# Optimization experiments

Hardware: AMD Instinct MI355X
Metric: run time of the kernel (lower is better)

## Reference

```python
import jax, jax.numpy as jnp
import numpy as np

B, T, F, D, NH, HD, WIN = 4, 512, 32, 128, 4, 32, 64
HIDDEN = 4 * D


def _ln(x, g, b, eps=1e-5):
    m = x.mean(-1, keepdims=True)
    v = ((x - m) ** 2).mean(-1, keepdims=True)
    return (x - m) / jnp.sqrt(v + eps) * g + b


def _rope(x):
    # x: [N, T, NH, HD] -- identical rotary applied to every head (matches per-head loop)
    hd = x.shape[-1]
    inv_freq = 1.0 / (10000.0 ** (jnp.arange(0, hd, 2, dtype=jnp.float32) / hd))
    t = jnp.arange(x.shape[1], dtype=jnp.float32)
    fr = t[:, None] * inv_freq                      # [T, HD/2]
    sin = jnp.sin(fr)[None, :, None, :]
    cos = jnp.cos(fr)[None, :, None, :]
    xe, xo = x[..., 0::2], x[..., 1::2]
    re = xe * cos - xo * sin
    ro = xe * sin + xo * cos
    return jnp.stack([re, ro], axis=-1).reshape(x.shape)


def setup_inputs() -> dict:
    key = jax.random.key(0)
    ks = jax.random.split(key, 8)
    s = 0.05
    return {
        "x": jax.random.normal(ks[0], (B, T, F), jnp.float32),
        "W_in": jax.random.normal(ks[1], (D, F), jnp.float32) * s,
        "b_in": jnp.zeros((D,), jnp.float32),
        "gamma1": jnp.ones((D,), jnp.float32),
        "beta1": jnp.zeros((D,), jnp.float32),
        "gamma2": jnp.ones((D,), jnp.float32),
        "beta2": jnp.zeros((D,), jnp.float32),
        "W_qkv": jax.random.normal(ks[2], (3 * D, D), jnp.float32) * s,
        "b_qkv": jnp.zeros((3 * D,), jnp.float32),
        "W_o": jax.random.normal(ks[3], (D, D), jnp.float32) * s,
        "b_o": jnp.zeros((D,), jnp.float32),
        "W1": jax.random.normal(ks[4], (HIDDEN, D), jnp.float32) * s,
        "b1": jnp.zeros((HIDDEN,), jnp.float32),
        "W2": jax.random.normal(ks[5], (D, HIDDEN), jnp.float32) * s,
        "b2": jnp.zeros((D,), jnp.float32),
        "W_out": jax.random.normal(ks[6], (F, D), jnp.float32) * s,
        "b_out": jnp.zeros((F,), jnp.float32),
    }


def reference(x, W_in, b_in, gamma1, beta1, gamma2, beta2, W_qkv, b_qkv,
              W_o, b_o, W1, b1, W2, b2, W_out, b_out):
    Bb, Tt, Ff = x.shape
    # channel-independent projection: hcf[b,f,t,:] = x[b,t,f] * W_in[:,f] + b_in
    hcf = jnp.einsum('btf,df->bftd', x, W_in) + b_in        # [B,F,T,D]
    hcf = hcf.reshape(Bb * Ff, Tt, D)                       # [BF,T,D]
    h1 = _ln(hcf, gamma1, beta1)
    # RoPE on q,k BEFORE the attention's internal qkv projection (as in source)
    qk = _rope(h1.reshape(Bb * Ff, Tt, NH, HD)).reshape(Bb * Ff, Tt, D)
    Wq, Wk, Wv = jnp.split(W_qkv, 3, axis=0)
    bq, bk, bv = jnp.split(b_qkv, 3)
    Q = (qk @ Wq.T + bq).reshape(-1, Tt, NH, HD)
    K = (qk @ Wk.T + bk).reshape(-1, Tt, NH, HD)
    V = (h1 @ Wv.T + bv).reshape(-1, Tt, NH, HD)
    i = jnp.arange(Tt)
    allowed = (i[None, :] <= i[:, None]) & ((i[:, None] - i[None, :]) <= WIN)
    mask = jnp.where(allowed, 0.0, -jnp.inf)                # [T,T]
    scores = jnp.einsum('bthd,bshd->bhts', Q, K) / jnp.sqrt(jnp.float32(HD)) + mask
    p = jax.nn.softmax(scores, axis=-1)
    o = jnp.einsum('bhts,bshd->bthd', p, V).reshape(-1, Tt, D)
    y = o @ W_o.T + b_o
    h2 = hcf + y
    h3 = _ln(h2, gamma2, beta2)
    ffn = jax.nn.gelu(h3 @ W1.T + b1, approximate=False) @ W2.T + b2
    h4 = h2 + ffn
    y_out = h4.reshape(Bb, Ff, Tt, D).mean(-1).transpose(0, 2, 1)   # [B,T,F]
    y_proj = (x @ W_in.T + b_in) @ W_out.T + b_out                   # [B,T,F]
    return x + y_out + y_proj
```

## Files before the change

kernel.cpp:

```cpp
#include <hip/hip_runtime.h>
#include <hip/hip_bf16.h>

typedef unsigned short u16;
typedef unsigned int u32;
typedef __attribute__((ext_vector_type(8))) short bf16x8;
typedef __attribute__((ext_vector_type(4))) float f32x4;
typedef __attribute__((ext_vector_type(4))) unsigned short u16x4;
typedef __attribute__((ext_vector_type(2))) unsigned int u32x2;

static constexpr int TSEQ = 512;
static constexpr int NSEQ = 128;
static constexpr int NTOK = NSEQ * TSEQ;

__device__ __forceinline__ float bf2f(u16 u) {
  u32 i = ((u32)u) << 16; float f; __builtin_memcpy(&f, &i, 4); return f;
}
__device__ __forceinline__ u16 f2bf(float f) {
  u32 u; __builtin_memcpy(&u, &f, 4);
  return (u16)((u + 0x7FFFu + ((u >> 16) & 1u)) >> 16);
}
__device__ __forceinline__ f32x4 mfma16(bf16x8 a, bf16x8 b, f32x4 c) {
  return __builtin_amdgcn_mfma_f32_16x16x32_bf16(a, b, c, 0, 0, 0);
}
__device__ __forceinline__ void gload_lds16(const u16* g, u16* l) {
  __builtin_amdgcn_global_load_lds((const __attribute__((address_space(1))) void*)g,
                                   (__attribute__((address_space(3))) void*)l, 16, 0, 0);
}
__device__ __forceinline__ float gelu_t(float v) {
  float uu = 0.7978845608f * (v + 0.044715f * v * v * v);
  return v / (1.f + __expf(-2.f * uu));
}

__global__ void k0_prep(const float* __restrict__ Wqkv, const float* __restrict__ Wo,
                        const float* __restrict__ W1, const float* __restrict__ W2,
                        const float* __restrict__ b2,
                        u16* __restrict__ Wqkv_b, u16* __restrict__ Wo_b,
                        u16* __restrict__ W1_b, float* __restrict__ cm,
                        float* __restrict__ b2m,
                        float* __restrict__ rc, float* __restrict__ rs) {
  int i = blockIdx.x * 256 + threadIdx.x;
  if (i < 49152) Wqkv_b[i] = f2bf(Wqkv[i]);
  if (i < 16384) Wo_b[i] = f2bf(Wo[i]);
  if (i < 65536) W1_b[i] = f2bf(W1[i]);
  if (i < 512) {
    float s = 0.f;
    for (int d = 0; d < 128; ++d) s += W2[d * 512 + i];
    cm[i] = s * (1.f / 128.f);
  }
  if (i == 0) {
    float s = 0.f;
    for (int d = 0; d < 128; ++d) s += b2[d];
    *b2m = s * (1.f / 128.f);
  }
  if (i < 8192) {
    int t = i >> 4, fi = i & 15;
    float inv = powf(10000.f, -(float)(2 * fi) / 32.f);
    float ang = (float)t * inv;
    rc[i] = cosf(ang); rs[i] = sinf(ang);
  }
}

__global__ void k1_embed(const float* __restrict__ x, const float* __restrict__ W_in,
                         const float* __restrict__ b_in,
                         const float* __restrict__ g1, const float* __restrict__ be1,
                         u16* __restrict__ hcf, u16* __restrict__ h1, u16* __restrict__ qk,
                         const float* __restrict__ rc, const float* __restrict__ rs) {
  int w = threadIdx.x >> 6, l = threadIdx.x & 63;
  int n = blockIdx.x * 4 + w;
  int t = n & (TSEQ - 1), seq = n >> 9;
  int f = seq & 31, b = seq >> 5;
  float xv = x[((b << 9) + t) * 32 + f];
  int d0 = l * 2;
  float v0 = xv * W_in[d0 * 32 + f] + b_in[d0];
  float v1 = xv * W_in[(d0 + 1) * 32 + f] + b_in[d0 + 1];
  float s = v0 + v1, ss = v0 * v0 + v1 * v1;
  #pragma unroll
  for (int m = 1; m < 64; m <<= 1) { s += __shfl_xor(s, m); ss += __shfl_xor(ss, m); }
  float mean = s * (1.f / 128.f);
  float var = ss * (1.f / 128.f) - mean * mean;
  float rstd = rsqrtf(var + 1e-5f);
  float a0 = (v0 - mean) * rstd * g1[d0] + be1[d0];
  float a1 = (v1 - mean) * rstd * g1[d0 + 1] + be1[d0 + 1];
  ((u32*)hcf)[n * 64 + l] = (u32)f2bf(v0) | ((u32)f2bf(v1) << 16);
  ((u32*)h1)[n * 64 + l]  = (u32)f2bf(a0) | ((u32)f2bf(a1) << 16);
  float c = rc[t * 16 + (l & 15)], sn = rs[t * 16 + (l & 15)];
  float re = a0 * c - a1 * sn, ro = a0 * sn + a1 * c;
  ((u32*)qk)[n * 64 + l] = (u32)f2bf(re) | ((u32)f2bf(ro) << 16);
}

__global__ __launch_bounds__(512, 4)
void gemm_qkv(const u16* __restrict__ QKin, const u16* __restrict__ H1,
              const u16* __restrict__ Wqkv, const float* __restrict__ bqkv,
              u16* __restrict__ QKb, u16* __restrict__ Vb) {
  __shared__ u16 Aq[64 * 128];
  __shared__ u16 Ah[64 * 128];
  const int tid = threadIdx.x, l = tid & 63, w = tid >> 6;
  const int lr = l & 15, lg = l >> 4;
  const int m0 = blockIdx.x * 64;
  const int wb = __builtin_amdgcn_readfirstlane(tid & 0x1C0);

  #pragma unroll
  for (int it = 0; it < 2; ++it) {
    int ci = it * 512 + tid;
    int row = ci >> 4, p = ci & 15;
    size_t goff = (size_t)(m0 + row) * 128 + ((p ^ (row & 7)) << 3);
    gload_lds16(QKin + goff, Aq + (size_t)(it * 512 + wb) * 8);
    gload_lds16(H1 + goff, Ah + (size_t)(it * 512 + wb) * 8);
  }
  __syncthreads();

  #pragma unroll 1
  for (int ph = 0; ph < 3; ++ph) {
    const u16* As = (ph == 2) ? Ah : Aq;
    const int wrow = ph * 128 + w * 16;
    const u16* wr = Wqkv + (size_t)(wrow + lr) * 128 + lg * 8;
    bf16x8 wf0 = *(const bf16x8*)(wr);
    bf16x8 wf1 = *(const bf16x8*)(wr + 32);
    bf16x8 wf2 = *(const bf16x8*)(wr + 64);
    bf16x8 wf3 = *(const bf16x8*)(wr + 96);
    f32x4 bs = *(const f32x4*)(bqkv + wrow + lg * 4);
    u16* C = (ph == 2) ? Vb : QKb;
    const int ldc = (ph == 2) ? 128 : 256;
    const int ccol = ((ph == 2) ? 0 : ph * 128) + w * 16 + lg * 4;
    #pragma unroll
    for (int tt = 0; tt < 4; ++tt) {
      const int tok = tt * 16 + lr;
      const u16* ar = As + (tok * 16) * 8;
      f32x4 a0 = mfma16(wf0, *(const bf16x8*)(ar + ((lg ^ (lr & 7)) << 3)),
                        (f32x4){0.f, 0.f, 0.f, 0.f});
      a0 = mfma16(wf1, *(const bf16x8*)(ar + (((4 + lg) ^ (lr & 7)) << 3)), a0);
      f32x4 a1 = mfma16(wf2, *(const bf16x8*)(ar + (((8 + lg) ^ (lr & 7)) << 3)),
                        (f32x4){0.f, 0.f, 0.f, 0.f});
      a1 = mfma16(wf3, *(const bf16x8*)(ar + (((12 + lg) ^ (lr & 7)) << 3)), a1);
      f32x4 a = a0 + a1;
      u16x4 qv;
      #pragma unroll
      for (int r = 0; r < 4; ++r) qv[r] = f2bf(a[r] + bs[r]);
      *(u16x4*)(C + (size_t)(m0 + tok) * ldc + ccol) = qv;
    }
    __builtin_amdgcn_sched_barrier(0);
  }
}

__global__ __launch_bounds__(512, 4)
void wo_ln_ffn(const u16* __restrict__ OB, const u16* __restrict__ Wo_b,
               const float* __restrict__ bo, const u16* __restrict__ HCF,
               const float* __restrict__ g2, const float* __restrict__ be2,
               const u16* __restrict__ W1b, const float* __restrict__ b1,
               const float* __restrict__ cm, const float* __restrict__ b2m,
               float* __restrict__ yout) {
  __shared__ u16 Buf[64 * 136];
  __shared__ float Sm[64 * 8], Sq[64 * 8];
  __shared__ float Yp[64 * 8];
  __shared__ float Hm[64];
  const int tid = threadIdx.x, l = tid & 63, w = tid >> 6;
  const int lr = l & 15, lg = l >> 4;
  const int m0 = blockIdx.x * 64;
  const int wb = __builtin_amdgcn_readfirstlane(tid & 0x1C0);

  #pragma unroll
  for (int it = 0; it < 2; ++it) {
    int ci = it * 512 + tid;
    int row = ci >> 4, p = ci & 15;
    gload_lds16(OB + (size_t)(m0 + row) * 128 + ((p ^ (row & 7)) << 3),
                Buf + (size_t)(it * 512 + wb) * 8);
  }
  __syncthreads();

  const int wrow = w * 16;
  {
    const u16* wr0 = Wo_b + (size_t)(wrow + lr) * 128 + lg * 8;
    bf16x8 wf0 = *(const bf16x8*)(wr0);
    bf16x8 wf1 = *(const bf16x8*)(wr0 + 32);
    bf16x8 wf2 = *(const bf16x8*)(wr0 + 64);
    bf16x8 wf3 = *(const bf16x8*)(wr0 + 96);
    f32x4 bs = *(const f32x4*)(bo + wrow + lg * 4);
    f32x4 hv[4];
    #pragma unroll
    for (int tt = 0; tt < 4; ++tt) {
      const int tok = tt * 16 + lr;
      const u16* ar = Buf + (tok * 16) * 8;
      f32x4 a0 = mfma16(wf0, *(const bf16x8*)(ar + ((lg ^ (lr & 7)) << 3)),
                        (f32x4){0.f, 0.f, 0.f, 0.f});
      a0 = mfma16(wf1, *(const bf16x8*)(ar + (((4 + lg) ^ (lr & 7)) << 3)), a0);
      f32x4 a1 = mfma16(wf2, *(const bf16x8*)(ar + (((8 + lg) ^ (lr & 7)) << 3)),
                        (f32x4){0.f, 0.f, 0.f, 0.f});
      a1 = mfma16(wf3, *(const bf16x8*)(ar + (((12 + lg) ^ (lr & 7)) << 3)), a1);
      f32x4 a = a0 + a1;
      u16x4 rv = *(const u16x4*)(HCF + (size_t)(m0 + tok) * 128 + wrow + lg * 4);
      #pragma unroll
      for (int r = 0; r < 4; ++r) hv[tt][r] = a[r] + bs[r] + bf2f(rv[r]);
    }
    #pragma unroll
    for (int tt = 0; tt < 4; ++tt) {
      float psm = hv[tt][0] + hv[tt][1] + hv[tt][2] + hv[tt][3];
      float psq = hv[tt][0] * hv[tt][0] + hv[tt][1] * hv[tt][1]
                + hv[tt][2] * hv[tt][2] + hv[tt][3] * hv[tt][3];
      psm += __shfl_xor(psm, 16); psq += __shfl_xor(psq, 16);
      psm += __shfl_xor(psm, 32); psq += __shfl_xor(psq, 32);
      if (lg == 0) { Sm[(tt * 16 + lr) * 8 + w] = psm; Sq[(tt * 16 + lr) * 8 + w] = psq; }
    }
    __syncthreads();
    f32x4 gm = *(const f32x4*)(g2 + wrow + lg * 4);
    f32x4 bt = *(const f32x4*)(be2 + wrow + lg * 4);
    #pragma unroll
    for (int tt = 0; tt < 4; ++tt) {
      const int tok = tt * 16 + lr;
      float s = 0.f, q = 0.f;
      #pragma unroll
      for (int ww = 0; ww < 8; ++ww) { s += Sm[tok * 8 + ww]; q += Sq[tok * 8 + ww]; }
      float mean = s * (1.f / 128.f);
      float var = q * (1.f / 128.f) - mean * mean;
      float rstd = rsqrtf(var + 1e-5f);
      if (w == 0 && lg == 0) Hm[tok] = mean;
      u16x4 qv;
      #pragma unroll
      for (int r = 0; r < 4; ++r)
        qv[r] = f2bf((hv[tt][r] - mean) * rstd * gm[r] + bt[r]);
      *(u16x4*)(Buf + tok * 136 + wrow + lg * 4) = qv;
    }
  }
  __syncthreads();

  float yacc[4] = {0.f, 0.f, 0.f, 0.f};
  #pragma unroll 1
  for (int p = 0; p < 4; ++p) {
    const int hb = (p * 8 + w) * 16;
    const u16* wr = W1b + (size_t)(hb + lr) * 128 + lg * 8;
    bf16x8 wf0 = *(const bf16x8*)(wr);
    bf16x8 wf1 = *(const bf16x8*)(wr + 32);
    bf16x8 wf2 = *(const bf16x8*)(wr + 64);
    bf16x8 wf3 = *(const bf16x8*)(wr + 96);
    f32x4 cmv = *(const f32x4*)(cm + hb + lg * 4);
    f32x4 bsv = *(const f32x4*)(b1 + hb + lg * 4);
    #pragma unroll
    for (int tt = 0; tt < 4; ++tt) {
      const u16* ar = Buf + (tt * 16 + lr) * 136 + lg * 8;
      f32x4 a0 = mfma16(wf0, *(const bf16x8*)(ar), (f32x4){0.f, 0.f, 0.f, 0.f});
      a0 = mfma16(wf1, *(const bf16x8*)(ar + 32), a0);
      f32x4 a1 = mfma16(wf2, *(const bf16x8*)(ar + 64), (f32x4){0.f, 0.f, 0.f, 0.f});
      a1 = mfma16(wf3, *(const bf16x8*)(ar + 96), a1);
      f32x4 a = a0 + a1;
      #pragma unroll
      for (int r = 0; r < 4; ++r)
        yacc[tt] += cmv[r] * gelu_t(a[r] + bsv[r]);
    }
    __builtin_amdgcn_sched_barrier(0);
  }

  #pragma unroll
  for (int tt = 0; tt < 4; ++tt) {
    float p = yacc[tt];
    p += __shfl_xor(p, 16);
    p += __shfl_xor(p, 32);
    if (lg == 0) Yp[(tt * 16 + lr) * 8 + w] = p;
  }
  __syncthreads();
  if (tid < 64) {
    float s = 0.f;
    #pragma unroll
    for (int ww = 0; ww < 8; ++ww) s += Yp[tid * 8 + ww];
    yout[m0 + tid] = Hm[tid] + b2m[0] + s;
  }
}

__global__ __launch_bounds__(256, 4)
void attn_mfma(const u16* __restrict__ QK, const u16* __restrict__ V, u16* __restrict__ O) {
  __shared__ u16 Ks[192 * 32];
  __shared__ u16 Vt[32 * 192];
  __shared__ u16 Pl[4][16 * 96];
  const int qstart = blockIdx.x * 128, seq = blockIdx.y, h = blockIdx.z;
  const int tid = threadIdx.x, w = tid >> 6, l = tid & 63;
  const int lr = l & 15, lg = l >> 4;
  const size_t base = (size_t)seq * TSEQ;

  #pragma unroll
  for (int it = 0; it < 3; ++it) {
    int idx = it * 256 + tid;
    int kl = idx >> 2, c = idx & 3;
    int kg = qstart - 64 + kl; if (kg < 0) kg = 0;
    bf16x8 kv = *(const bf16x8*)(QK + (base + kg) * 256 + 128 + h * 32 + c * 8);
    int pc = c ^ ((kl >> 1) & 3);
    *(bf16x8*)(Ks + kl * 32 + pc * 8) = kv;
    bf16x8 vv = *(const bf16x8*)(V + (base + kg) * 128 + h * 32 + c * 8);
    #pragma unroll
    for (int j = 0; j < 8; ++j) {
      int hd = c * 8 + j;
      int f = ((hd & 7) ^ (hd >> 3)) & 7;
      Vt[hd * 192 + (((kl >> 3) ^ f) * 8) + (kl & 7)] = (u16)vv[j];
    }
  }
  __syncthreads();

  const float scale = 0.17677669529663687f;
  for (int qt = 0; qt < 2; ++qt) {
    const int klbase = (w * 2 + qt) * 16;
    const int t0 = qstart + klbase;
    bf16x8 qf = *(const bf16x8*)(QK + (base + t0 + lr) * 256 + h * 32 + lg * 8);
    f32x4 s[5];
    #pragma unroll
    for (int kt = 0; kt < 5; ++kt) {
      int key = klbase + kt * 16 + lr;
      int pc = lg ^ ((key >> 1) & 3);
      bf16x8 kf = *(const bf16x8*)(Ks + key * 32 + pc * 8);
      s[kt] = mfma16(kf, qf, (f32x4){0.f, 0.f, 0.f, 0.f});
    }
    float m = -1e30f;
    #pragma unroll
    for (int kt = 0; kt < 5; ++kt)
      #pragma unroll
      for (int r = 0; r < 4; ++r) {
        int kl = kt * 16 + lg * 4 + r;
        bool valid = (kl >= lr) && (kl <= lr + 64) && (kl >= 64 - t0);
        float sv = valid ? s[kt][r] * scale : -1e30f;
        s[kt][r] = sv;
        m = fmaxf(m, sv);
      }
    m = fmaxf(m, __shfl_xor(m, 16));
    m = fmaxf(m, __shfl_xor(m, 32));
    float sum = 0.f;
    #pragma unroll
    for (int kt = 0; kt < 5; ++kt)
      #pragma unroll
      for (int r = 0; r < 4; ++r) { float p = __expf(s[kt][r] - m); s[kt][r] = p; sum += p; }
    sum += __shfl_xor(sum, 16);
    sum += __shfl_xor(sum, 32);
    float rinv = 1.f / sum;
    u16* P = Pl[w];
    #pragma unroll
    for (int kt = 0; kt < 5; ++kt) {
      u32 lo = (u32)f2bf(s[kt][0] * rinv) | ((u32)f2bf(s[kt][1] * rinv) << 16);
      u32 hi = (u32)f2bf(s[kt][2] * rinv) | ((u32)f2bf(s[kt][3] * rinv) << 16);
      int u = 2 * kt + (lg >> 1);
      int up = (u & ~3) | ((u & 3) ^ (lr & 3));
      *(u32x2*)(P + lr * 96 + up * 8 + (lg & 1) * 4) = (u32x2){lo, hi};
    }
    {
      int u = 10 + (lg >> 1);
      int up = (u & ~3) | ((u & 3) ^ (lr & 3));
      *(u32x2*)(P + lr * 96 + up * 8 + (lg & 1) * 4) = (u32x2){0u, 0u};
    }
    f32x4 acc[2] = {{0.f,0.f,0.f,0.f},{0.f,0.f,0.f,0.f}};
    #pragma unroll
    for (int c = 0; c < 3; ++c) {
      int u = 4 * c + (lg ^ (lr & 3));
      bf16x8 pf = *(const bf16x8*)(P + lr * 96 + u * 8);
      #pragma unroll
      for (int n = 0; n < 2; ++n) {
        int hd = n * 16 + lr;
        int f = ((hd & 7) ^ (hd >> 3)) & 7;
        int uv = (klbase >> 3) + 4 * c + lg; if (uv > 23) uv = 23;
        bf16x8 vf = *(const bf16x8*)(Vt + hd * 192 + ((uv ^ f) * 8));
        acc[n] = mfma16(pf, vf, acc[n]);
      }
    }
    #pragma unroll
    for (int n = 0; n < 2; ++n)
      #pragma unroll
      for (int r = 0; r < 4; ++r)
        O[(base + t0 + lg * 4 + r) * 128 + h * 32 + n * 16 + lr] = f2bf(acc[n][r]);
  }
}

__global__ void k7_out(const float* __restrict__ x, const float* __restrict__ W_in,
                       const float* __restrict__ b_in, const float* __restrict__ Wout,
                       const float* __restrict__ bout, const float* __restrict__ yout,
                       float* __restrict__ out) {
  __shared__ float mids[4][128];
  int w = threadIdx.x >> 6, l = threadIdx.x & 63;
  int p = blockIdx.x * 4 + w;
  int b = p >> 9, t = p & 511;
  const float* xr = x + (size_t)p * 32;
  float m0 = b_in[2 * l], m1 = b_in[2 * l + 1];
  #pragma unroll
  for (int f = 0; f < 32; ++f) {
    float xv = xr[f];
    m0 += xv * W_in[(2 * l) * 32 + f];
    m1 += xv * W_in[(2 * l + 1) * 32 + f];
  }
  mids[w][2 * l] = m0; mids[w][2 * l + 1] = m1;
  __syncthreads();
  if (l < 32) {
    float a = bout[l];
    #pragma unroll 16
    for (int dd = 0; dd < 128; ++dd) a += mids[w][dd] * Wout[l * 128 + dd];
    float yo = yout[((b * 32 + l) << 9) + t];
    out[(size_t)p * 32 + l] = xr[l] + yo + a;
  }
}

extern "C" void kernel_launch(void* const* d_in, const int* in_sizes, int n_in,
                              void* d_out, int out_size, void* d_ws, size_t ws_size,
                              hipStream_t stream) {
  const float* x    = (const float*)d_in[0];
  const float* W_in = (const float*)d_in[1];
  const float* b_in = (const float*)d_in[2];
  const float* g1   = (const float*)d_in[3];
  const float* be1  = (const float*)d_in[4];
  const float* g2   = (const float*)d_in[5];
  const float* be2  = (const float*)d_in[6];
  const float* Wqkv = (const float*)d_in[7];
  const float* bqkv = (const float*)d_in[8];
  const float* Wo   = (const float*)d_in[9];
  const float* bo   = (const float*)d_in[10];
  const float* W1   = (const float*)d_in[11];
  const float* b1   = (const float*)d_in[12];
  const float* W2   = (const float*)d_in[13];
  const float* b2   = (const float*)d_in[14];
  const float* Wout = (const float*)d_in[15];
  const float* bout = (const float*)d_in[16];
  float* out = (float*)d_out;

  char* ws = (char*)d_ws;
  size_t off = 0;
  auto alloc = [&](size_t bytes) -> void* {
    void* p = ws + off; off += (bytes + 1023) & ~(size_t)1023; return p;
  };
  float* rc     = (float*)alloc(512 * 16 * 4);
  float* rs     = (float*)alloc(512 * 16 * 4);
  u16* Wqkv_b   = (u16*)alloc(49152 * 2);
  u16* Wo_b     = (u16*)alloc(16384 * 2);
  u16* W1_b     = (u16*)alloc(65536 * 2);
  float* cm     = (float*)alloc(512 * 4);
  float* b2m    = (float*)alloc(4);
  float* yout   = (float*)alloc((size_t)NTOK * 4);
  u16* hcf      = (u16*)alloc((size_t)NTOK * 128 * 2);
  u16* obuf     = (u16*)alloc((size_t)NTOK * 128 * 2);
  u16* h1       = (u16*)alloc((size_t)NTOK * 128 * 2);
  u16* qk       = (u16*)alloc((size_t)NTOK * 128 * 2);
  u16* QKb      = (u16*)alloc((size_t)NTOK * 256 * 2);
  u16* Vb       = (u16*)alloc((size_t)NTOK * 128 * 2);

  k0_prep<<<dim3(256), dim3(256), 0, stream>>>(Wqkv, Wo, W1, W2, b2,
                                               Wqkv_b, Wo_b, W1_b, cm, b2m, rc, rs);
  k1_embed<<<dim3(NTOK / 4), dim3(256), 0, stream>>>(x, W_in, b_in, g1, be1, hcf, h1, qk, rc, rs);
  gemm_qkv<<<dim3(1024), dim3(512), 0, stream>>>(qk, h1, Wqkv_b, bqkv, QKb, Vb);
  attn_mfma<<<dim3(4, 128, 4), dim3(256), 0, stream>>>(QKb, Vb, obuf);
  wo_ln_ffn<<<dim3(1024), dim3(512), 0, stream>>>(obuf, Wo_b, bo, hcf, g2, be2,
                                                  W1_b, b1, cm, b2m, yout);
  k7_out<<<dim3(512), dim3(256), 0, stream>>>(x, W_in, b_in, Wout, bout, yout, out);
}
```

Before: 137.1 us.

## Fuse embed+LN1+RoPE into QKV GEMM and fold W_in·W_out for output

The separate embedding/LayerNorm/RoPE kernel is merged into the QKV GEMM. Each block now computes its 64 tokens' hcf, h1 and rotated qk in registers and writes them straight into swizzled LDS, so the h1 and qk intermediates no longer round-trip through global memory. The output kernel also uses a precomputed 32x32 matrix Wout·W_in and bias in place of the two-stage 128-wide projection. This removes a launch and about 32 MB of intermediate traffic, at the cost of more register pressure and serial prologue work inside the GEMM blocks.

```diff
diff --git a/kernel.cpp b/kernel.cpp
--- a/kernel.cpp
+++ b/kernel.cpp
@@ -4,9 +4,9 @@
 typedef unsigned short u16;
 typedef unsigned int u32;
 typedef __attribute__((ext_vector_type(8))) short bf16x8;
+typedef __attribute__((ext_vector_type(8))) unsigned short u16x8;
 typedef __attribute__((ext_vector_type(4))) float f32x4;
 typedef __attribute__((ext_vector_type(4))) unsigned short u16x4;
-typedef __attribute__((ext_vector_type(2))) unsigned int u32x2;
 
 static constexpr int TSEQ = 512;
 static constexpr int NSEQ = 128;
@@ -34,9 +34,12 @@
 __global__ void k0_prep(const float* __restrict__ Wqkv, const float* __restrict__ Wo,
                         const float* __restrict__ W1, const float* __restrict__ W2,
                         const float* __restrict__ b2,
+                        const float* __restrict__ W_in, const float* __restrict__ b_in,
+                        const float* __restrict__ Wout, const float* __restrict__ bout,
                         u16* __restrict__ Wqkv_b, u16* __restrict__ Wo_b,
                         u16* __restrict__ W1_b, float* __restrict__ cm,
                         float* __restrict__ b2m,
+                        float* __restrict__ Wcomb, float* __restrict__ bcomb,
                         float* __restrict__ rc, float* __restrict__ rs) {
   int i = blockIdx.x * 256 + threadIdx.x;
   if (i < 49152) Wqkv_b[i] = f2bf(Wqkv[i]);
@@ -52,6 +55,17 @@
     for (int d = 0; d < 128; ++d) s += b2[d];
     *b2m = s * (1.f / 128.f);
   }
+  if (i < 1024) {
+    int l = i >> 5, f = i & 31;
+    float s = 0.f;
+    for (int d = 0; d < 128; ++d) s += Wout[l * 128 + d] * W_in[d * 32 + f];
+    Wcomb[i] = s;
+  }
+  if (i < 32) {
+    float s = bout[i];
+    for (int d = 0; d < 128; ++d) s += Wout[i * 128 + d] * b_in[d];
+    bcomb[i] = s;
+  }
   if (i < 8192) {
     int t = i >> 4, fi = i & 15;
     float inv = powf(10000.f, -(float)(2 * fi) / 32.f);
@@ -60,52 +74,63 @@
   }
 }
 
-__global__ void k1_embed(const float* __restrict__ x, const float* __restrict__ W_in,
-                         const float* __restrict__ b_in,
-                         const float* __restrict__ g1, const float* __restrict__ be1,
-                         u16* __restrict__ hcf, u16* __restrict__ h1, u16* __restrict__ qk,
-                         const float* __restrict__ rc, const float* __restrict__ rs) {
-  int w = threadIdx.x >> 6, l = threadIdx.x & 63;
-  int n = blockIdx.x * 4 + w;
-  int t = n & (TSEQ - 1), seq = n >> 9;
-  int f = seq & 31, b = seq >> 5;
-  float xv = x[((b << 9) + t) * 32 + f];
-  int d0 = l * 2;
-  float v0 = xv * W_in[d0 * 32 + f] + b_in[d0];
-  float v1 = xv * W_in[(d0 + 1) * 32 + f] + b_in[d0 + 1];
-  float s = v0 + v1, ss = v0 * v0 + v1 * v1;
-  #pragma unroll
-  for (int m = 1; m < 64; m <<= 1) { s += __shfl_xor(s, m); ss += __shfl_xor(ss, m); }
-  float mean = s * (1.f / 128.f);
-  float var = ss * (1.f / 128.f) - mean * mean;
-  float rstd = rsqrtf(var + 1e-5f);
-  float a0 = (v0 - mean) * rstd * g1[d0] + be1[d0];
-  float a1 = (v1 - mean) * rstd * g1[d0 + 1] + be1[d0 + 1];
-  ((u32*)hcf)[n * 64 + l] = (u32)f2bf(v0) | ((u32)f2bf(v1) << 16);
-  ((u32*)h1)[n * 64 + l]  = (u32)f2bf(a0) | ((u32)f2bf(a1) << 16);
-  float c = rc[t * 16 + (l & 15)], sn = rs[t * 16 + (l & 15)];
-  float re = a0 * c - a1 * sn, ro = a0 * sn + a1 * c;
-  ((u32*)qk)[n * 64 + l] = (u32)f2bf(re) | ((u32)f2bf(ro) << 16);
-}
-
 __global__ __launch_bounds__(512, 4)
-void gemm_qkv(const u16* __restrict__ QKin, const u16* __restrict__ H1,
-              const u16* __restrict__ Wqkv, const float* __restrict__ bqkv,
-              u16* __restrict__ QKb, u16* __restrict__ Vb) {
+void embed_qkv(const float* __restrict__ x, const float* __restrict__ W_in,
+               const float* __restrict__ b_in,
+               const float* __restrict__ g1, const float* __restrict__ be1,
+               const float* __restrict__ rc, const float* __restrict__ rs,
+               const u16* __restrict__ Wqkv, const float* __restrict__ bqkv,
+               u16* __restrict__ hcf, u16* __restrict__ QKb, u16* __restrict__ Vb) {
   __shared__ u16 Aq[64 * 128];
   __shared__ u16 Ah[64 * 128];
   const int tid = threadIdx.x, l = tid & 63, w = tid >> 6;
   const int lr = l & 15, lg = l >> 4;
   const int m0 = blockIdx.x * 64;
-  const int wb = __builtin_amdgcn_readfirstlane(tid & 0x1C0);
-
-  #pragma unroll
-  for (int it = 0; it < 2; ++it) {
-    int ci = it * 512 + tid;
-    int row = ci >> 4, p = ci & 15;
-    size_t goff = (size_t)(m0 + row) * 128 + ((p ^ (row & 7)) << 3);
-    gload_lds16(QKin + goff, Aq + (size_t)(it * 512 + wb) * 8);
-    gload_lds16(H1 + goff, Ah + (size_t)(it * 512 + wb) * 8);
+  const int seq = m0 >> 9, f = seq & 31, b = seq >> 5, tbase = m0 & 511;
+
+  {
+    const int tok = tid >> 3, j = tid & 7, d0 = j * 16;
+    const int t = tbase + tok;
+    float xv = x[((b << 9) + t) * 32 + f];
+    float hc[16], av[16];
+    float s = 0.f, ss = 0.f;
+    #pragma unroll
+    for (int m = 0; m < 16; ++m) {
+      float v = xv * W_in[(d0 + m) * 32 + f] + b_in[d0 + m];
+      hc[m] = v; s += v; ss += v * v;
+    }
+    s += __shfl_xor(s, 1); ss += __shfl_xor(ss, 1);
+    s += __shfl_xor(s, 2); ss += __shfl_xor(ss, 2);
+    s += __shfl_xor(s, 4); ss += __shfl_xor(ss, 4);
+    float mean = s * (1.f / 128.f);
+    float var = ss * (1.f / 128.f) - mean * mean;
+    float rstd = rsqrtf(var + 1e-5f);
+    #pragma unroll
+    for (int m = 0; m < 16; ++m)
+      av[m] = (hc[m] - mean) * rstd * g1[d0 + m] + be1[d0 + m];
+    u16x8 hv0, hv1;
+    #pragma unroll
+    for (int m = 0; m < 8; ++m) { hv0[m] = f2bf(hc[m]); hv1[m] = f2bf(hc[8 + m]); }
+    *(u16x8*)(hcf + (size_t)(m0 + tok) * 128 + d0) = hv0;
+    *(u16x8*)(hcf + (size_t)(m0 + tok) * 128 + d0 + 8) = hv1;
+    u16x8 ah0, ah1, aq0, aq1;
+    #pragma unroll
+    for (int m = 0; m < 8; ++m) { ah0[m] = f2bf(av[m]); ah1[m] = f2bf(av[8 + m]); }
+    #pragma unroll
+    for (int m = 0; m < 8; ++m) {
+      int i16 = ((d0 >> 1) + m) & 15;
+      float c = rc[t * 16 + i16], sn = rs[t * 16 + i16];
+      float re = av[2 * m] * c - av[2 * m + 1] * sn;
+      float ro = av[2 * m] * sn + av[2 * m + 1] * c;
+      if (m < 4) { aq0[2 * m] = f2bf(re); aq0[2 * m + 1] = f2bf(ro); }
+      else { aq1[2 * (m - 4)] = f2bf(re); aq1[2 * (m - 4) + 1] = f2bf(ro); }
+    }
+    const int p0 = j * 2;
+    const int s0 = p0 ^ (tok & 7), s1 = (p0 + 1) ^ (tok & 7);
+    *(u16x8*)(Ah + (tok * 16 + s0) * 8) = ah0;
+    *(u16x8*)(Ah + (tok * 16 + s1) * 8) = ah1;
+    *(u16x8*)(Aq + (tok * 16 + s0) * 8) = aq0;
+    *(u16x8*)(Aq + (tok * 16 + s1) * 8) = aq1;
   }
   __syncthreads();
 
@@ -269,6 +294,7 @@
   __shared__ u16 Ks[192 * 32];
   __shared__ u16 Vt[32 * 192];
   __shared__ u16 Pl[4][16 * 96];
+  typedef __attribute__((ext_vector_type(2))) unsigned int u32x2;
   const int qstart = blockIdx.x * 128, seq = blockIdx.y, h = blockIdx.z;
   const int tid = threadIdx.x, w = tid >> 6, l = tid & 63;
   const int lr = l & 15, lg = l >> 4;
@@ -362,31 +388,27 @@
   }
 }
 
-__global__ void k7_out(const float* __restrict__ x, const float* __restrict__ W_in,
-                       const float* __restrict__ b_in, const float* __restrict__ Wout,
-                       const float* __restrict__ bout, const float* __restrict__ yout,
+__global__ void k7_out(const float* __restrict__ x, const float* __restrict__ Wcomb,
+                       const float* __restrict__ bcomb, const float* __restrict__ yout,
                        float* __restrict__ out) {
-  __shared__ float mids[4][128];
-  int w = threadIdx.x >> 6, l = threadIdx.x & 63;
-  int p = blockIdx.x * 4 + w;
-  int b = p >> 9, t = p & 511;
-  const float* xr = x + (size_t)p * 32;
-  float m0 = b_in[2 * l], m1 = b_in[2 * l + 1];
+  __shared__ float Wc[32 * 33];
+  __shared__ float bc[32];
+  const int tid = threadIdx.x;
+  for (int i = tid; i < 1024; i += 256) Wc[(i >> 5) * 33 + (i & 31)] = Wcomb[i];
+  if (tid < 32) bc[tid] = bcomb[tid];
+  __syncthreads();
+  const int p = blockIdx.x * 8 + (tid >> 5);
+  const int l = tid & 31;
+  const int bb = p >> 9, t = p & 511;
+  float xv = x[(size_t)p * 32 + l];
+  float acc = bc[l];
   #pragma unroll
-  for (int f = 0; f < 32; ++f) {
-    float xv = xr[f];
-    m0 += xv * W_in[(2 * l) * 32 + f];
-    m1 += xv * W_in[(2 * l + 1) * 32 + f];
-  }
-  mids[w][2 * l] = m0; mids[w][2 * l + 1] = m1;
-  __syncthreads();
-  if (l < 32) {
-    float a = bout[l];
-    #pragma unroll 16
-    for (int dd = 0; dd < 128; ++dd) a += mids[w][dd] * Wout[l * 128 + dd];
-    float yo = yout[((b * 32 + l) << 9) + t];
-    out[(size_t)p * 32 + l] = xr[l] + yo + a;
-  }
+  for (int ff = 0; ff < 32; ++ff) {
+    float xf = __shfl(xv, ff, 32);
+    acc += xf * Wc[l * 33 + ff];
+  }
+  float yo = yout[((bb * 32 + l) << 9) + t];
+  out[(size_t)p * 32 + l] = xv + yo + acc;
 }
 
 extern "C" void kernel_launch(void* const* d_in, const int* in_sizes, int n_in,
@@ -423,20 +445,22 @@
   u16* W1_b     = (u16*)alloc(65536 * 2);
   float* cm     = (float*)alloc(512 * 4);
   float* b2m    = (float*)alloc(4);
+  float* Wcomb  = (float*)alloc(1024 * 4);
+  float* bcomb  = (float*)alloc(32 * 4);
   float* yout   = (float*)alloc((size_t)NTOK * 4);
   u16* hcf      = (u16*)alloc((size_t)NTOK * 128 * 2);
   u16* obuf     = (u16*)alloc((size_t)NTOK * 128 * 2);
-  u16* h1       = (u16*)alloc((size_t)NTOK * 128 * 2);
-  u16* qk       = (u16*)alloc((size_t)NTOK * 128 * 2);
   u16* QKb      = (u16*)alloc((size_t)NTOK * 256 * 2);
   u16* Vb       = (u16*)alloc((size_t)NTOK * 128 * 2);
 
   k0_prep<<<dim3(256), dim3(256), 0, stream>>>(Wqkv, Wo, W1, W2, b2,
-                                               Wqkv_b, Wo_b, W1_b, cm, b2m, rc, rs);
-  k1_embed<<<dim3(NTOK / 4), dim3(256), 0, stream>>>(x, W_in, b_in, g1, be1, hcf, h1, qk, rc, rs);
-  gemm_qkv<<<dim3(1024), dim3(512), 0, stream>>>(qk, h1, Wqkv_b, bqkv, QKb, Vb);
+                                               W_in, b_in, Wout, bout,
+                                               Wqkv_b, Wo_b, W1_b, cm, b2m,
+                                               Wcomb, bcomb, rc, rs);
+  embed_qkv<<<dim3(1024), dim3(512), 0, stream>>>(x, W_in, b_in, g1, be1, rc, rs,
+                                                  Wqkv_b, bqkv, hcf, QKb, Vb);
   attn_mfma<<<dim3(4, 128, 4), dim3(256), 0, stream>>>(QKb, Vb, obuf);
   wo_ln_ffn<<<dim3(1024), dim3(512), 0, stream>>>(obuf, Wo_b, bo, hcf, g2, be2,
                                                   W1_b, b1, cm, b2m, yout);
-  k7_out<<<dim3(512), dim3(256), 0, stream>>>(x, W_in, b_in, Wout, bout, yout, out);
-}
+  k7_out<<<dim3(256), dim3(256), 0, stream>>>(x, Wcomb, bcomb, yout, out);
+}
```

After: 119.2 us. -13.1%, faster.
